# Kernel tuning notes

Hardware: AMD Instinct MI355X
Metric: run time of the kernel (lower is better)

The kernel has to match this reference:

```python
import jax, jax.numpy as jnp
import numpy as np
import math

FACTOR = 5

def setup_inputs() -> dict:
    key = jax.random.key(0)
    kq, kk, kv = jax.random.split(key, 3)
    B, L, H, D = 2, 4096, 8, 64
    queries = jax.random.normal(kq, (B, L, H, D), dtype=jnp.float32)
    keys = jax.random.normal(kk, (B, L, H, D), dtype=jnp.float32)
    values = jax.random.normal(kv, (B, L, H, D), dtype=jnp.float32)
    attn_mask = jnp.ones((B, L), dtype=jnp.int32)
    return {"queries": queries, "keys": keys, "values": values, "attn_mask": attn_mask}

def reference(queries, keys, values, attn_mask):
    B, L_Q, H, D = queries.shape
    L_K = keys.shape[1]
    # [B, L, H, D] -> [B, H, L, D]
    Q = jnp.transpose(queries, (0, 2, 1, 3))
    K = jnp.transpose(keys, (0, 2, 1, 3))
    V = jnp.transpose(values, (0, 2, 1, 3))

    U_part = max(min(FACTOR * int(math.ceil(math.log(max(L_K, 1)))), L_K), 1)
    u = max(min(FACTOR * int(math.ceil(math.log(max(L_Q, 1)))), L_Q), 1)

    # random key sampling per query (torch.randint replaced by fixed jax key)
    idx = jax.random.randint(jax.random.key(1), (L_Q, U_part), 0, L_K)  # [L_Q, S]
    K_sample = K[:, :, idx, :]  # [B, H, L_Q, S, D]  (irregular gather)
    Q_K_sample = jnp.einsum('bhqd,bhqsd->bhqs', Q, K_sample)  # [B, H, L_Q, S]

    # sparsity measure M = max - mean(full-length normalization L_K as in source)
    M = Q_K_sample.max(axis=-1) - Q_K_sample.sum(axis=-1) / L_K  # [B, H, L_Q]
    _, M_top = jax.lax.top_k(M, u)  # [B, H, u]

    Q_reduce = jnp.take_along_axis(Q, M_top[..., None], axis=2)  # [B, H, u, D]
    scale = 1.0 / math.sqrt(D)
    scores = jnp.einsum('bhud,bhkd->bhuk', Q_reduce, K) * scale  # [B, H, u, L_K]

    mask = attn_mask[:, None, None, :]  # [B,1,1,L_K]
    scores = jnp.where(mask == 0, -jnp.inf, scores)

    A = jax.nn.softmax(scores, axis=-1)  # dropout p=0 -> identity
    context = jnp.einsum('bhuk,bhkd->bhud', A, V)  # [B, H, u, D]
    return jnp.transpose(context, (0, 2, 1, 3))  # [B, u, H, D]
```

## Files before the change

### kernel.cpp

```cpp
#include <hip/hip_runtime.h>
#include <math.h>

#define JAX_PARTITIONABLE 1

constexpr int Bc = 2, Lc = 4096, Hc = 8, Dc = 64;
constexpr int BHc = Bc * Hc;
constexpr int Uc = 45;
constexpr int NSc = 45;

struct TF2 { unsigned a, b; };

__host__ __device__ constexpr unsigned rotl32(unsigned v, int n) {
  return (v << n) | (v >> (32 - n));
}

__host__ __device__ constexpr TF2 tf2(unsigned k0, unsigned k1, unsigned x0, unsigned x1) {
  unsigned ks2 = k0 ^ k1 ^ 0x1BD11BDAu;
  x0 += k0; x1 += k1;
  x0 += x1; x1 = rotl32(x1, 13); x1 ^= x0;
  x0 += x1; x1 = rotl32(x1, 15); x1 ^= x0;
  x0 += x1; x1 = rotl32(x1, 26); x1 ^= x0;
  x0 += x1; x1 = rotl32(x1, 6);  x1 ^= x0;
  x0 += k1; x1 += ks2 + 1u;
  x0 += x1; x1 = rotl32(x1, 17); x1 ^= x0;
  x0 += x1; x1 = rotl32(x1, 29); x1 ^= x0;
  x0 += x1; x1 = rotl32(x1, 16); x1 ^= x0;
  x0 += x1; x1 = rotl32(x1, 24); x1 ^= x0;
  x0 += ks2; x1 += k0 + 2u;
  x0 += x1; x1 = rotl32(x1, 13); x1 ^= x0;
  x0 += x1; x1 = rotl32(x1, 15); x1 ^= x0;
  x0 += x1; x1 = rotl32(x1, 26); x1 ^= x0;
  x0 += x1; x1 = rotl32(x1, 6);  x1 ^= x0;
  x0 += k0; x1 += k1 + 3u;
  x0 += x1; x1 = rotl32(x1, 17); x1 ^= x0;
  x0 += x1; x1 = rotl32(x1, 29); x1 ^= x0;
  x0 += x1; x1 = rotl32(x1, 16); x1 ^= x0;
  x0 += x1; x1 = rotl32(x1, 24); x1 ^= x0;
  x0 += k1; x1 += ks2 + 4u;
  x0 += x1; x1 = rotl32(x1, 13); x1 ^= x0;
  x0 += x1; x1 = rotl32(x1, 15); x1 ^= x0;
  x0 += x1; x1 = rotl32(x1, 26); x1 ^= x0;
  x0 += x1; x1 = rotl32(x1, 6);  x1 ^= x0;
  x0 += ks2; x1 += k0 + 5u;
  return TF2{x0, x1};
}

__global__ __launch_bounds__(256) void k_idx(int* __restrict__ idx) {
  int f = blockIdx.x * 256 + threadIdx.x;
  constexpr TF2 kb = tf2(0u, 1u, 0u, 1u);
  TF2 r = tf2(kb.a, kb.b, 0u, (unsigned)f);
  idx[f] = (int)((r.a ^ r.b) & 4095u);
}

__global__ __launch_bounds__(256) void k_scoreM(const float* __restrict__ Q, const float* __restrict__ K,
                                                const int* __restrict__ idx, float* __restrict__ M) {
  __shared__ float sp[720 * 5];
  __shared__ float ps[720];
  __shared__ int sidx[720];
  int tid = threadIdx.x;
  int bx = blockIdx.x;
  int bh = bx & 15;
  int qblk = bx >> 4;
  int b = bh >> 3, h = bh & 7;
  int lane16 = tid & 15, qloc = tid >> 4;
  int q = qblk * 16 + qloc;
  for (int e = tid; e < 720; e += 256) sidx[e] = idx[qblk * 720 + e];
  __syncthreads();
  const float4* Q4 = (const float4*)Q;
  const float4* K4 = (const float4*)K;
  float4 qr = Q4[((b * Lc + q) * Hc + h) * 16 + lane16];
  int kbase = (b * Lc * Hc + h) * 16 + lane16;
  const int* ip = sidx + qloc * NSc;
  float* wr = sp + (qloc * NSc) * 5 + (lane16 >> 2);
  bool wlane = (lane16 & 3) == 0;
  #pragma unroll 9
  for (int s = 0; s < NSc; ++s) {
    int kk = ip[s];
    float4 kv = K4[kbase + kk * (Hc * 16)];
    float p = qr.x * kv.x + qr.y * kv.y + qr.z * kv.z + qr.w * kv.w;
    p += __shfl_xor(p, 1);
    p += __shfl_xor(p, 2);
    if (wlane) wr[s * 5] = p;
  }
  __syncthreads();
  for (int p = tid; p < 720; p += 256) {
    const float* r = sp + p * 5;
    ps[p] = (r[0] + r[1]) + (r[2] + r[3]);
  }
  __syncthreads();
  if (tid < 16) {
    const float* r = ps + tid * NSc;
    float mx = r[0], sm = r[0];
    for (int s = 1; s < NSc; ++s) { float v = r[s]; mx = fmaxf(mx, v); sm += v; }
    M[bh * Lc + qblk * 16 + tid] = mx - sm * (1.0f / Lc);
  }
}

__global__ __launch_bounds__(256) void k_topk(const float* __restrict__ M, int* __restrict__ topk) {
  __shared__ unsigned su[Lc];
  __shared__ int hist[256];
  __shared__ int sfx[257];
  __shared__ unsigned s_prefix;
  __shared__ int s_r;
  __shared__ int n_gt, n_eq;
  __shared__ unsigned cu[64];
  __shared__ int cidx[64];
  __shared__ int eqi[64];
  int bh = blockIdx.x, tid = threadIdx.x;
  const float* m = M + bh * Lc;
  for (int e = tid; e < Lc; e += 256) {
    unsigned bb = __float_as_uint(m[e]);
    su[e] = (bb & 0x80000000u) ? ~bb : (bb | 0x80000000u);
  }
  if (tid == 0) { s_r = Uc; s_prefix = 0u; n_gt = 0; n_eq = 0; }
  __syncthreads();
  #pragma unroll
  for (int p = 0; p < 4; ++p) {
    int shift = 24 - 8 * p;
    hist[tid] = 0;
    __syncthreads();
    unsigned pref = s_prefix;
    unsigned hmask = (p == 0) ? 0u : (0xFFFFFFFFu << (shift + 8));
    for (int e = tid; e < Lc; e += 256) {
      unsigned u = su[e];
      if ((u & hmask) == pref) atomicAdd(&hist[(u >> shift) & 255u], 1);
    }
    __syncthreads();
    sfx[tid] = hist[tid];
    __syncthreads();
    for (int off = 1; off < 256; off <<= 1) {
      int v = (tid + off < 256) ? sfx[tid + off] : 0;
      __syncthreads();
      sfx[tid] += v;
      __syncthreads();
    }
    int r = s_r;
    __syncthreads();
    int above = (tid < 255) ? sfx[tid + 1] : 0;
    if (sfx[tid] >= r && above < r) {
      s_r = r - above;
      s_prefix = pref | ((unsigned)tid << shift);
    }
    __syncthreads();
  }
  unsigned T = s_prefix;
  int rf = s_r;
  for (int e = tid; e < Lc; e += 256) {
    unsigned u = su[e];
    if (u > T) {
      int p = atomicAdd(&n_gt, 1);
      cu[p] = u; cidx[p] = e;
    } else if (u == T) {
      int p = atomicAdd(&n_eq, 1);
      if (p < 64) eqi[p] = e;
    }
  }
  __syncthreads();
  int ne = n_eq < 64 ? n_eq : 64;
  if (tid < ne) {
    int myi = eqi[tid];
    int rank = 0;
    for (int j = 0; j < ne; ++j) rank += (eqi[j] < myi);
    if (rank < rf) {
      int p = atomicAdd(&n_gt, 1);
      cu[p] = T; cidx[p] = myi;
    }
  }
  __syncthreads();
  if (tid < Uc) {
    unsigned mu = cu[tid]; int mi = cidx[tid];
    int rank = 0;
    for (int j = 0; j < Uc; ++j) {
      unsigned ju = cu[j]; int ji = cidx[j];
      rank += (ju > mu) || (ju == mu && ji < mi);
    }
    topk[bh * Uc + rank] = mi;
  }
}

template<int NC>
__global__ __launch_bounds__(256) void k_attn(const float* __restrict__ Q, const float* __restrict__ K,
                                              const float* __restrict__ V, const int* __restrict__ amask,
                                              const int* __restrict__ topk,
                                              float* __restrict__ pO, float* __restrict__ pM,
                                              float* __restrict__ pL) {
  constexpr int CH = Lc / NC;
  constexpr int TG = 256 / CH;
  int chunk = blockIdx.x, bh = blockIdx.y;
  int b = bh >> 3, h = bh & 7;
  int tid = threadIdx.x;
  __shared__ int tk[Uc];
  __shared__ __align__(16) float qs[Uc * 64];
  __shared__ float sc[48][CH + 1];
  if (tid < Uc) tk[tid] = topk[bh * Uc + tid];
  __syncthreads();
  for (int e = tid; e < Uc * 64; e += 256) {
    int t = e >> 6, d = e & 63;
    qs[e] = Q[((b * Lc + tk[t]) * Hc + h) * Dc + d];
  }
  for (int e = tid; e < 3 * CH; e += 256) sc[45 + e / CH][e % CH] = 0.f;
  __syncthreads();
  {
    int k = tid % CH, tg = tid / CH;
    int key = chunk * CH + k;
    const float4* K4 = (const float4*)K;
    int kb = ((b * Lc + key) * Hc + h) * 16;
    float4 kr[16];
    #pragma unroll
    for (int j = 0; j < 16; ++j) kr[j] = K4[kb + j];
    int mk = amask[b * Lc + key];
    const float4* qs4 = (const float4*)qs;
    for (int t = tg; t < Uc; t += TG) {
      float acc = 0.f;
      #pragma unroll
      for (int j = 0; j < 16; ++j) {
        float4 qv = qs4[t * 16 + j];
        acc += qv.x * kr[j].x;
        acc += qv.y * kr[j].y;
        acc += qv.z * kr[j].z;
        acc += qv.w * kr[j].w;
      }
      sc[t][k] = mk ? acc * 0.125f : -INFINITY;
    }
  }
  __syncthreads();
  {
    constexpr int COLS = CH / 64;
    int w = tid >> 6, lane = tid & 63;
    for (int t = w; t < Uc; t += 4) {
      float x[COLS];
      float ml = -INFINITY;
      #pragma unroll
      for (int c = 0; c < COLS; ++c) { x[c] = sc[t][c * 64 + lane]; ml = fmaxf(ml, x[c]); }
      #pragma unroll
      for (int off = 1; off < 64; off <<= 1) ml = fmaxf(ml, __shfl_xor(ml, off));
      float ls = 0.f;
      if (ml != -INFINITY) {
        #pragma unroll
        for (int c = 0; c < COLS; ++c) { x[c] = __expf(x[c] - ml); ls += x[c]; }
      } else {
        #pragma unroll
        for (int c = 0; c < COLS; ++c) x[c] = 0.f;
      }
      #pragma unroll
      for (int c = 0; c < COLS; ++c) sc[t][c * 64 + lane] = x[c];
      #pragma unroll
      for (int off = 1; off < 64; off <<= 1) ls += __shfl_xor(ls, off);
      if (lane == 0) {
        pM[(bh * NC + chunk) * Uc + t] = ml;
        pL[(bh * NC + chunk) * Uc + t] = ls;
      }
    }
  }
  __syncthreads();
  {
    int ty = tid >> 4, tx = tid & 15;
    float4 o0 = {0.f, 0.f, 0.f, 0.f};
    float4 o1 = {0.f, 0.f, 0.f, 0.f};
    float4 o2 = {0.f, 0.f, 0.f, 0.f};
    const float4* V4 = (const float4*)V;
    int vbase = (b * Lc + chunk * CH) * (Hc * 16) + h * 16 + tx;
    #pragma unroll 4
    for (int k = 0; k < CH; ++k) {
      float4 v4 = V4[vbase + k * (Hc * 16)];
      float p0 = sc[ty][k], p1 = sc[ty + 16][k], p2 = sc[ty + 32][k];
      o0.x += p0 * v4.x; o0.y += p0 * v4.y; o0.z += p0 * v4.z; o0.w += p0 * v4.w;
      o1.x += p1 * v4.x; o1.y += p1 * v4.y; o1.z += p1 * v4.z; o1.w += p1 * v4.w;
      o2.x += p2 * v4.x; o2.y += p2 * v4.y; o2.z += p2 * v4.z; o2.w += p2 * v4.w;
    }
    float4* pO4 = (float4*)pO;
    int obase = ((bh * NC + chunk) * Uc) * 16 + tx;
    pO4[obase + ty * 16] = o0;
    pO4[obase + (ty + 16) * 16] = o1;
    if (ty < 13) pO4[obase + (ty + 32) * 16] = o2;
  }
}

template<int NC>
__global__ __launch_bounds__(256) void k_merge(const float* __restrict__ pO, const float* __restrict__ pM,
                                               const float* __restrict__ pL, float* __restrict__ out) {
  int f = blockIdx.x * 256 + threadIdx.x;
  int d = f & 63, h = (f >> 6) & 7;
  int bt = f >> 9;
  int t = bt % Uc, b = bt / Uc;
  int bh = b * 8 + h;
  float m = -INFINITY;
  for (int c = 0; c < NC; ++c) m = fmaxf(m, pM[(bh * NC + c) * Uc + t]);
  float den = 0.f, num = 0.f;
  for (int c = 0; c < NC; ++c) {
    float mc = pM[(bh * NC + c) * Uc + t];
    float wgt = (mc == -INFINITY) ? 0.f : __expf(mc - m);
    den += wgt * pL[(bh * NC + c) * Uc + t];
    num += wgt * pO[((bh * NC + c) * Uc + t) * 64 + d];
  }
  out[f] = num / den;
}

extern "C" void kernel_launch(void* const* d_in, const int* in_sizes, int n_in,
                              void* d_out, int out_size, void* d_ws, size_t ws_size,
                              hipStream_t stream) {
  const float* Q = (const float*)d_in[0];
  const float* K = (const float*)d_in[1];
  const float* V = (const float*)d_in[2];
  const int* amask = (const int*)d_in[3];
  float* out = (float*)d_out;
  char* ws = (char*)d_ws;
  int*   idx  = (int*)(ws + 0x000000);
  float* M    = (float*)(ws + 0x0B4000);
  int*   topk = (int*)(ws + 0x0F4000);
  float* pM   = (float*)(ws + 0x101000);
  size_t need64 = 0x101000UL + 64UL * 190080UL;
  size_t need32 = 0x101000UL + 32UL * 190080UL;
  int NC = ws_size >= need64 ? 64 : (ws_size >= need32 ? 32 : 16);
  float* pL = pM + 16 * NC * Uc;
  float* pO = pL + 16 * NC * Uc;

  k_idx<<<720, 256, 0, stream>>>(idx);
  k_scoreM<<<4096, 256, 0, stream>>>(Q, K, idx, M);
  k_topk<<<BHc, 256, 0, stream>>>(M, topk);
  if (NC == 64) {
    k_attn<64><<<dim3(64, BHc), 256, 0, stream>>>(Q, K, V, amask, topk, pO, pM, pL);
    k_merge<64><<<180, 256, 0, stream>>>(pO, pM, pL, out);
  } else if (NC == 32) {
    k_attn<32><<<dim3(32, BHc), 256, 0, stream>>>(Q, K, V, amask, topk, pO, pM, pL);
    k_merge<32><<<180, 256, 0, stream>>>(pO, pM, pL, out);
  } else {
    k_attn<16><<<dim3(16, BHc), 256, 0, stream>>>(Q, K, V, amask, topk, pO, pM, pL);
    k_merge<16><<<180, 256, 0, stream>>>(pO, pM, pL, out);
  }
}
```

Baseline: 184.8 us.

## Fuse index generation into scoring, batch gathers, pre-gather top-k queries

Removes the separate random-index kernel and computes the threefry indices inline inside the scoring kernel, so one launch and the idx buffer round trip go away. The sampled-key loop is restructured to issue five gathered loads before using them, giving more memory-level parallelism. The top-k kernel now also gathers the selected query rows into a compact buffer, which the attention blocks copy with float4 loads instead of each block doing a scattered gather. This adds redundant hash work per scoring block and extra register use.

```diff
diff --git a/kernel.cpp b/kernel.cpp
--- a/kernel.cpp
+++ b/kernel.cpp
@@ -45,15 +45,8 @@
   return TF2{x0, x1};
 }
 
-__global__ __launch_bounds__(256) void k_idx(int* __restrict__ idx) {
-  int f = blockIdx.x * 256 + threadIdx.x;
-  constexpr TF2 kb = tf2(0u, 1u, 0u, 1u);
-  TF2 r = tf2(kb.a, kb.b, 0u, (unsigned)f);
-  idx[f] = (int)((r.a ^ r.b) & 4095u);
-}
-
 __global__ __launch_bounds__(256) void k_scoreM(const float* __restrict__ Q, const float* __restrict__ K,
-                                                const int* __restrict__ idx, float* __restrict__ M) {
+                                                float* __restrict__ M) {
   __shared__ float sp[720 * 5];
   __shared__ float ps[720];
   __shared__ int sidx[720];
@@ -64,7 +57,11 @@
   int b = bh >> 3, h = bh & 7;
   int lane16 = tid & 15, qloc = tid >> 4;
   int q = qblk * 16 + qloc;
-  for (int e = tid; e < 720; e += 256) sidx[e] = idx[qblk * 720 + e];
+  constexpr TF2 kb = tf2(0u, 1u, 0u, 1u);
+  for (int e = tid; e < 720; e += 256) {
+    TF2 r = tf2(kb.a, kb.b, 0u, (unsigned)(qblk * 720 + e));
+    sidx[e] = (int)((r.a ^ r.b) & 4095u);
+  }
   __syncthreads();
   const float4* Q4 = (const float4*)Q;
   const float4* K4 = (const float4*)K;
@@ -73,14 +70,21 @@
   const int* ip = sidx + qloc * NSc;
   float* wr = sp + (qloc * NSc) * 5 + (lane16 >> 2);
   bool wlane = (lane16 & 3) == 0;
-  #pragma unroll 9
-  for (int s = 0; s < NSc; ++s) {
-    int kk = ip[s];
-    float4 kv = K4[kbase + kk * (Hc * 16)];
-    float p = qr.x * kv.x + qr.y * kv.y + qr.z * kv.z + qr.w * kv.w;
-    p += __shfl_xor(p, 1);
-    p += __shfl_xor(p, 2);
-    if (wlane) wr[s * 5] = p;
+  #pragma unroll
+  for (int s0 = 0; s0 < NSc; s0 += 5) {
+    int kk[5];
+    #pragma unroll
+    for (int i = 0; i < 5; ++i) kk[i] = ip[s0 + i];
+    float4 kv[5];
+    #pragma unroll
+    for (int i = 0; i < 5; ++i) kv[i] = K4[kbase + kk[i] * (Hc * 16)];
+    #pragma unroll
+    for (int i = 0; i < 5; ++i) {
+      float p = qr.x * kv[i].x + qr.y * kv[i].y + qr.z * kv[i].z + qr.w * kv[i].w;
+      p += __shfl_xor(p, 1);
+      p += __shfl_xor(p, 2);
+      if (wlane) wr[(s0 + i) * 5] = p;
+    }
   }
   __syncthreads();
   for (int p = tid; p < 720; p += 256) {
@@ -96,7 +100,8 @@
   }
 }
 
-__global__ __launch_bounds__(256) void k_topk(const float* __restrict__ M, int* __restrict__ topk) {
+__global__ __launch_bounds__(256) void k_topk(const float* __restrict__ M, const float* __restrict__ Q,
+                                              int* __restrict__ topk, float* __restrict__ qg) {
   __shared__ unsigned su[Lc];
   __shared__ int hist[256];
   __shared__ int sfx[257];
@@ -106,7 +111,9 @@
   __shared__ unsigned cu[64];
   __shared__ int cidx[64];
   __shared__ int eqi[64];
+  __shared__ int srank[Uc];
   int bh = blockIdx.x, tid = threadIdx.x;
+  int b = bh >> 3, h = bh & 7;
   const float* m = M + bh * Lc;
   for (int e = tid; e < Lc; e += 256) {
     unsigned bb = __float_as_uint(m[e]);
@@ -175,13 +182,20 @@
       rank += (ju > mu) || (ju == mu && ji < mi);
     }
     topk[bh * Uc + rank] = mi;
+    srank[rank] = mi;
+  }
+  __syncthreads();
+  const float4* Q4 = (const float4*)Q;
+  float4* qg4 = (float4*)qg;
+  for (int e = tid; e < Uc * 16; e += 256) {
+    int t = e >> 4, dq = e & 15;
+    qg4[bh * Uc * 16 + e] = Q4[((b * Lc + srank[t]) * Hc + h) * 16 + dq];
   }
 }
 
 template<int NC>
-__global__ __launch_bounds__(256) void k_attn(const float* __restrict__ Q, const float* __restrict__ K,
+__global__ __launch_bounds__(256) void k_attn(const float* __restrict__ qg, const float* __restrict__ K,
                                               const float* __restrict__ V, const int* __restrict__ amask,
-                                              const int* __restrict__ topk,
                                               float* __restrict__ pO, float* __restrict__ pM,
                                               float* __restrict__ pL) {
   constexpr int CH = Lc / NC;
@@ -189,14 +203,12 @@
   int chunk = blockIdx.x, bh = blockIdx.y;
   int b = bh >> 3, h = bh & 7;
   int tid = threadIdx.x;
-  __shared__ int tk[Uc];
   __shared__ __align__(16) float qs[Uc * 64];
   __shared__ float sc[48][CH + 1];
-  if (tid < Uc) tk[tid] = topk[bh * Uc + tid];
-  __syncthreads();
-  for (int e = tid; e < Uc * 64; e += 256) {
-    int t = e >> 6, d = e & 63;
-    qs[e] = Q[((b * Lc + tk[t]) * Hc + h) * Dc + d];
+  {
+    const float4* qg4 = (const float4*)qg;
+    float4* qs4w = (float4*)qs;
+    for (int e = tid; e < Uc * 16; e += 256) qs4w[e] = qg4[bh * Uc * 16 + e];
   }
   for (int e = tid; e < 3 * CH; e += 256) sc[45 + e / CH][e % CH] = 0.f;
   __syncthreads();
@@ -305,27 +317,26 @@
   const int* amask = (const int*)d_in[3];
   float* out = (float*)d_out;
   char* ws = (char*)d_ws;
-  int*   idx  = (int*)(ws + 0x000000);
-  float* M    = (float*)(ws + 0x0B4000);
-  int*   topk = (int*)(ws + 0x0F4000);
-  float* pM   = (float*)(ws + 0x101000);
-  size_t need64 = 0x101000UL + 64UL * 190080UL;
-  size_t need32 = 0x101000UL + 32UL * 190080UL;
+  float* M    = (float*)(ws + 0x000000);
+  int*   topk = (int*)(ws + 0x040000);
+  float* qg   = (float*)(ws + 0x041000);
+  float* pM   = (float*)(ws + 0x070000);
+  size_t need64 = 0x70000UL + 64UL * 190080UL;
+  size_t need32 = 0x70000UL + 32UL * 190080UL;
   int NC = ws_size >= need64 ? 64 : (ws_size >= need32 ? 32 : 16);
   float* pL = pM + 16 * NC * Uc;
   float* pO = pL + 16 * NC * Uc;
 
-  k_idx<<<720, 256, 0, stream>>>(idx);
-  k_scoreM<<<4096, 256, 0, stream>>>(Q, K, idx, M);
-  k_topk<<<BHc, 256, 0, stream>>>(M, topk);
+  k_scoreM<<<4096, 256, 0, stream>>>(Q, K, M);
+  k_topk<<<BHc, 256, 0, stream>>>(M, Q, topk, qg);
   if (NC == 64) {
-    k_attn<64><<<dim3(64, BHc), 256, 0, stream>>>(Q, K, V, amask, topk, pO, pM, pL);
+    k_attn<64><<<dim3(64, BHc), 256, 0, stream>>>(qg, K, V, amask, pO, pM, pL);
     k_merge<64><<<180, 256, 0, stream>>>(pO, pM, pL, out);
   } else if (NC == 32) {
-    k_attn<32><<<dim3(32, BHc), 256, 0, stream>>>(Q, K, V, amask, topk, pO, pM, pL);
+    k_attn<32><<<dim3(32, BHc), 256, 0, stream>>>(qg, K, V, amask, pO, pM, pL);
     k_merge<32><<<180, 256, 0, stream>>>(pO, pM, pL, out);
   } else {
-    k_attn<16><<<dim3(16, BHc), 256, 0, stream>>>(Q, K, V, amask, topk, pO, pM, pL);
+    k_attn<16><<<dim3(16, BHc), 256, 0, stream>>>(qg, K, V, amask, pO, pM, pL);
     k_merge<16><<<180, 256, 0, stream>>>(pO, pM, pL, out);
   }
 }
```

Measured after the change: 183.5 us. No clear change (-0.7%).
